# Kernel tuning notes

Measured on AMD Instinct MI355X. Metric: run time of the kernel, lower is better.

The kernel has to match this reference:

```python
import jax, jax.numpy as jnp
import numpy as np

B, T = 8, 512
ACT, EMB, DET, HID, NST = 32, 1024, 1024, 1024, 16
STO, CLS = 32, 32
UNIMIX = 0.01


def _ln(x, g, b):
    m = x.mean(-1, keepdims=True)
    v = x.var(-1, keepdims=True)
    return (x - m) / jnp.sqrt(v + 1e-5) * g + b


def _lnsilu(x, g, b):
    return jax.nn.silu(_ln(x, g, b))


def setup_inputs() -> dict:
    key = jax.random.key(0)
    ks = iter(jax.random.split(key, 40))

    def lin(din, dout):
        return jax.random.normal(next(ks), (din, dout), jnp.float32) / np.sqrt(din)

    actions = jax.random.normal(next(ks), (B, T, ACT), jnp.float32)
    embeds = jax.random.normal(next(ks), (B, T, EMB), jnp.float32)
    # pre_ssm: Linear(ACT,HID) + LayerNormSiLU(HID)
    W_pre, b_pre = lin(ACT, HID), jnp.zeros(HID)
    g_pre, bb_pre = jnp.ones(HID), jnp.zeros(HID)
    W_emb = lin(EMB, HID)  # bias=False
    W_in, b_in = lin(HID, 2 * DET), jnp.zeros(2 * DET)
    W_dt = lin(DET, DET)
    # dt bias init: inverse-softplus of dt ~ LogUniform(1e-3, 0.1)
    u = jax.random.uniform(next(ks), (DET,), jnp.float32)
    dt_init = jnp.exp(u * (np.log(0.1) - np.log(1e-3)) + np.log(1e-3))
    b_dt = dt_init + jnp.log(-jnp.expm1(-dt_init))
    W_B, W_C = lin(DET, NST), lin(DET, NST)
    A_log = jnp.broadcast_to(
        jnp.log(jnp.arange(1, NST + 1, dtype=jnp.float32)), (DET, NST)
    ) + jnp.zeros((DET, NST))
    Dp = jnp.ones(DET)
    g_out, b_out = jnp.ones(DET), jnp.zeros(DET)
    # prior_net: Linear(DET,HID)+LNSiLU+Linear(HID,STO*CLS)
    W_pr1, b_pr1 = lin(DET, HID), jnp.zeros(HID)
    g_pr, bb_pr = jnp.ones(HID), jnp.zeros(HID)
    W_pr2, b_pr2 = lin(HID, STO * CLS), jnp.zeros(STO * CLS)
    # post_net: Linear(DET+EMB,HID)+LNSiLU+Linear(HID,STO*CLS)
    W_po1, b_po1 = lin(DET + EMB, HID), jnp.zeros(HID)
    g_po, bb_po = jnp.ones(HID), jnp.zeros(HID)
    W_po2, b_po2 = lin(HID, STO * CLS), jnp.zeros(STO * CLS)
    return dict(actions=actions, embeds=embeds, W_pre=W_pre, b_pre=b_pre,
                g_pre=g_pre, bb_pre=bb_pre, W_emb=W_emb, W_in=W_in, b_in=b_in,
                W_dt=W_dt, b_dt=b_dt, W_B=W_B, W_C=W_C, A_log=A_log, Dp=Dp,
                g_out=g_out, b_out=b_out, W_pr1=W_pr1, b_pr1=b_pr1, g_pr=g_pr,
                bb_pr=bb_pr, W_pr2=W_pr2, b_pr2=b_pr2, W_po1=W_po1, b_po1=b_po1,
                g_po=g_po, bb_po=bb_po, W_po2=W_po2, b_po2=b_po2)


def reference(actions, embeds, W_pre, b_pre, g_pre, bb_pre, W_emb, W_in, b_in,
              W_dt, b_dt, W_B, W_C, A_log, Dp, g_out, b_out, W_pr1, b_pr1,
              g_pr, bb_pr, W_pr2, b_pr2, W_po1, b_po1, g_po, bb_po, W_po2, b_po2):
    # input projections
    x = _lnsilu(actions @ W_pre + b_pre, g_pre, bb_pre) + embeds @ W_emb  # (B,T,HID)
    x = x.transpose(1, 0, 2)  # (T,B,HID)
    xz = x @ W_in + b_in
    x_ssm, x_gate = xz[..., :DET], xz[..., DET:]
    dt = jax.nn.softplus(x_ssm @ W_dt + b_dt)        # (T,B,DET)
    Bp = x_ssm @ W_B                                  # (T,B,NST)
    Cp = x_ssm @ W_C                                  # (T,B,NST)
    A = -jnp.exp(A_log)                               # (DET,NST)
    gates = jnp.exp(dt[..., None] * A)                # (T,B,DET,NST)
    values = (dt * x_ssm)[..., None] * Bp[:, :, None, :]

    # linear recurrence h[t] = g[t]*h[t-1] + v[t] via associative scan
    def comb(a, c):
        g1, v1 = a
        g2, v2 = c
        return (g1 * g2, g2 * v1 + v2)

    _, h = jax.lax.associative_scan(comb, (gates, values), axis=0)
    y = jnp.einsum('tbdn,tbn->tbd', h, Cp) + Dp * x_ssm
    y = y * jax.nn.silu(x_gate)
    deter = _ln(y, g_out, b_out)                      # (T,B,DET)

    # prior / post heads
    prior = _lnsilu(deter @ W_pr1 + b_pr1, g_pr, bb_pr) @ W_pr2 + b_pr2
    emb_t = embeds.transpose(1, 0, 2)
    post_in = jnp.concatenate([deter, emb_t], -1)
    post = _lnsilu(post_in @ W_po1 + b_po1, g_po, bb_po) @ W_po2 + b_po2
    # unimix transform of post logits (deterministic part of _categorical)
    p = jax.nn.softmax(post.reshape(T, B, STO, CLS), -1)
    p = (1.0 - UNIMIX) * p + UNIMIX / CLS
    post_u = jnp.log(p + 1e-8).reshape(T, B, STO * CLS)
    return jnp.concatenate([deter, prior, post_u], -1)  # (T,B,DET+2*STO*CLS)
```

## Files before the change

kernel.cpp:

```cpp
#include <hip/hip_runtime.h>
#include <hip/hip_bf16.h>
#include <math.h>


typedef __bf16 bf16_t;
typedef __bf16 bf16x8 __attribute__((ext_vector_type(8)));
typedef float f32x4 __attribute__((ext_vector_type(4)));

#define B_   8
#define T_   512
#define R_   4096
#define HID_ 1024
#define NC_  16
#define CL_  32

static __device__ __forceinline__ float bf2f(bf16_t x) { return (float)x; }
static __device__ __forceinline__ bf16_t f2bf(float x) { return (bf16_t)x; }

typedef __attribute__((address_space(3))) unsigned int lds_u32;
typedef const __attribute__((address_space(1))) unsigned int glb_u32;
static __device__ __forceinline__ void gld16(const bf16_t* g, bf16_t* l) {
  __builtin_amdgcn_global_load_lds((glb_u32*)g, (lds_u32*)l, 16, 0, 0);
}

__global__ void detect_k(const unsigned int* __restrict__ dp_raw, int* __restrict__ flag) {
  if (threadIdx.x == 0) *flag = (dp_raw[0] == 0x3F803F80u) ? 1 : 0;
}

struct CvtArgs {
  const void* src[21];
  float* dst[21];
  int n[21];
};
__global__ __launch_bounds__(256) void cvt_vecs(CvtArgs a, const int* __restrict__ flag) {
  const bool isb = (*flag != 0);
  int v = blockIdx.y;
  const void* s = a.src[v];
  float* d = a.dst[v];
  int n = a.n[v];
  for (int i = blockIdx.x * 256 + threadIdx.x; i < n; i += 64 * 256)
    d[i] = isb ? bf2f(((const bf16_t*)s)[i]) : ((const float*)s)[i];
}

__device__ __forceinline__ void block_sum2(float& s, float& ss) {
#pragma unroll
  for (int off = 32; off > 0; off >>= 1) {
    s  += __shfl_down(s, off, 64);
    ss += __shfl_down(ss, off, 64);
  }
  __shared__ float red[8];
  int tid = threadIdx.x;
  int wave = tid >> 6, lane = tid & 63;
  if (lane == 0) { red[wave] = s; red[4 + wave] = ss; }
  __syncthreads();
  s  = red[0] + red[1] + red[2] + red[3];
  ss = red[4] + red[5] + red[6] + red[7];
}

__global__ void transpose_any(const void* __restrict__ src, bf16_t* __restrict__ dst,
                              int K, int N, const int* __restrict__ flag) {
  __shared__ float tile[32][33];
  const bool isb = (*flag != 0);
  int n0 = blockIdx.x * 32, k0 = blockIdx.y * 32;
  int tx = threadIdx.x, ty = threadIdx.y;
#pragma unroll
  for (int i = 0; i < 4; ++i) {
    size_t idx = (size_t)(k0 + ty + i * 8) * N + n0 + tx;
    tile[ty + i * 8][tx] = isb ? bf2f(((const bf16_t*)src)[idx]) : ((const float*)src)[idx];
  }
  __syncthreads();
#pragma unroll
  for (int i = 0; i < 4; ++i)
    dst[(size_t)(n0 + ty + i * 8) * K + k0 + tx] = f2bf(tile[tx][ty + i * 8]);
}

__global__ __launch_bounds__(256) void bc_build(const float* __restrict__ WB_f,
                                                const float* __restrict__ WC_f,
                                                bf16_t* __restrict__ WTbc) {
  int idx = blockIdx.x * 256 + threadIdx.x;
  int r = idx >> 10, k = idx & 1023;
  float v = 0.f;
  if (r < 16)      v = WB_f[k * 16 + r];
  else if (r < 32) v = WC_f[k * 16 + (r - 16)];
  WTbc[(size_t)r * 1024 + k] = f2bf(v);
}

__global__ __launch_bounds__(256) void reorder_emb(const void* __restrict__ emb,
                                                   bf16_t* __restrict__ embT,
                                                   const int* __restrict__ flag) {
  const bool isb = (*flag != 0);
  int r = blockIdx.x, tid = threadIdx.x;
  int t = r >> 3, b = r & 7;
  size_t base = (size_t)(b * T_ + t) * 1024;
#pragma unroll
  for (int i = 0; i < 4; ++i) {
    int c = i * 256 + tid;
    float v = isb ? bf2f(((const bf16_t*)emb)[base + c]) : ((const float*)emb)[base + c];
    embT[(size_t)r * 1024 + c] = f2bf(v);
  }
}

__global__ __launch_bounds__(256) void pre_kernel(
    const float* __restrict__ actions, const float* __restrict__ W_pre,
    const float* __restrict__ b_pre, const float* __restrict__ g_pre,
    const float* __restrict__ bb_pre, float* __restrict__ act_h) {
  int r = blockIdx.x, tid = threadIdx.x;
  int t = r >> 3, b = r & 7;
  __shared__ float a[32];
  if (tid < 32) a[tid] = actions[(size_t)(b * T_ + t) * 32 + tid];
  __syncthreads();
  float v[4];
  float s = 0.f, ss = 0.f;
#pragma unroll
  for (int i = 0; i < 4; ++i) {
    int n = i * 256 + tid;
    float acc = b_pre[n];
#pragma unroll
    for (int k = 0; k < 32; ++k) acc += a[k] * W_pre[k * HID_ + n];
    v[i] = acc; s += acc; ss += acc * acc;
  }
  block_sum2(s, ss);
  float mean = s * (1.f / 1024.f);
  float var  = ss * (1.f / 1024.f) - mean * mean;
  float rstd = rsqrtf(var + 1e-5f);
#pragma unroll
  for (int i = 0; i < 4; ++i) {
    int n = i * 256 + tid;
    float y = (v[i] - mean) * rstd * g_pre[n] + bb_pre[n];
    y = y / (1.f + __expf(-y));
    act_h[(size_t)r * HID_ + n] = y;
  }
}

enum { EPI_ADD_BF16 = 0, EPI_XZ = 1, EPI_SOFTPLUS = 2, EPI_BIAS_F32 = 3,
       EPI_PRIOR = 4, EPI_BC = 5 };

struct GemmArgs {
  const bf16_t* A;
  const bf16_t* Bt;
  int K;
  int N;
  int bnN;
  const float* bias;
  const float* addf;
  float* outf0;
  float* outf1;
  bf16_t* outh0;
  bf16_t* outh1;
  void* outv;
  const int* flag;
};

template <int EPI>
__global__ __launch_bounds__(256) void gemm_t(GemmArgs g) {
  __shared__ __align__(16) bf16_t As[64 * 32];
  __shared__ __align__(16) bf16_t Bs[64 * 32];
  const int tid = threadIdx.x;
  const int wave = tid >> 6, lane = tid & 63;
  const int K = g.K;

  const int per = gridDim.x >> 3;
  const int idx = (blockIdx.x & 7) * per + (blockIdx.x >> 3);
  const int bm = idx / g.bnN, bn = idx % g.bnN;

  f32x4 acc[2][2] = {};

  const int srow = tid >> 2;
  const int scol = (tid & 3) * 8;
  const bf16_t* Ap = g.A  + (size_t)(bm * 64 + srow) * K + scol;
  const bf16_t* Bp = g.Bt + (size_t)(bn * 64 + srow) * K + scol;
  bf16_t* AsW = &As[tid * 8];
  bf16_t* BsW = &Bs[tid * 8];

  const int wm = (wave >> 1) * 32, wn = (wave & 1) * 32;
  const int fm = lane & 15, fk = (lane >> 4) * 8;

  for (int k0 = 0; k0 < K; k0 += 32) {
    gld16(Ap + k0, AsW);
    gld16(Bp + k0, BsW);
    __syncthreads();
    bf16x8 af[2], bfr[2];
#pragma unroll
    for (int i = 0; i < 2; ++i)
      af[i] = *(const bf16x8*)&As[(wm + i * 16 + fm) * 32 + fk];
#pragma unroll
    for (int j = 0; j < 2; ++j)
      bfr[j] = *(const bf16x8*)&Bs[(wn + j * 16 + fm) * 32 + fk];
#pragma unroll
    for (int i = 0; i < 2; ++i)
#pragma unroll
      for (int j = 0; j < 2; ++j)
        acc[i][j] = __builtin_amdgcn_mfma_f32_16x16x32_bf16(af[i], bfr[j], acc[i][j], 0, 0, 0);
    __syncthreads();
  }

  const bool out_bf = (EPI == EPI_PRIOR) ? (*g.flag != 0) : false;
  const int em = (lane >> 4) * 4, en = lane & 15;
#pragma unroll
  for (int i = 0; i < 2; ++i) {
#pragma unroll
    for (int j = 0; j < 2; ++j) {
#pragma unroll
      for (int v = 0; v < 4; ++v) {
        int row = bm * 64 + wm + i * 16 + em + v;
        int col = bn * 64 + wn + j * 16 + en;
        float x = acc[i][j][v];
        if constexpr (EPI == EPI_ADD_BF16) {
          size_t o = (size_t)row * g.N + col;
          g.outh0[o] = f2bf(x + g.addf[o]);
        } else if constexpr (EPI == EPI_XZ) {
          float val = x + g.bias[col];
          if (col < 1024) {
            size_t o = (size_t)row * 1024 + col;
            g.outf0[o] = val;
            g.outh0[o] = f2bf(val);
          } else {
            size_t o = (size_t)row * 1024 + (col - 1024);
            g.outh1[o] = f2bf(val);
          }
        } else if constexpr (EPI == EPI_SOFTPLUS) {
          float val = x + g.bias[col];
          float sp = (val > 20.f) ? val : log1pf(__expf(val));
          g.outf0[(size_t)row * 1024 + col] = sp;
        } else if constexpr (EPI == EPI_BIAS_F32) {
          g.outf0[(size_t)row * g.N + col] = x + g.bias[col];
        } else if constexpr (EPI == EPI_BC) {
          if (col < 16)      g.outf0[(size_t)row * 16 + col] = x;
          else if (col < 32) g.outf1[(size_t)row * 16 + (col - 16)] = x;
        } else {
          float val = x + g.bias[col];
          size_t o = (size_t)row * 3072 + 1024 + col;
          if (out_bf) ((bf16_t*)g.outv)[o] = f2bf(val);
          else        ((float*)g.outv)[o]  = val;
        }
      }
    }
  }
}

__global__ __launch_bounds__(256) void scan_p1(const float* __restrict__ dt,
                                               const float* __restrict__ xs,
                                               const float* __restrict__ Bp,
                                               const float* __restrict__ A_log,
                                               float* __restrict__ Gp,
                                               float* __restrict__ Hl) {
  int idx = blockIdx.x * 256 + threadIdx.x;
  int d = idx & 1023;
  int cb = idx >> 10;
  int b = cb & 7, c = cb >> 3;
  float Ad[16];
#pragma unroll
  for (int n = 0; n < 16; ++n) Ad[n] = -__expf(A_log[d * 16 + n]);
  float h[16] = {};
  float dts = 0.f;
  int r0 = c * CL_ * 8 + b;
  for (int tl = 0; tl < CL_; ++tl) {
    int r = r0 + tl * 8;
    size_t off = (size_t)r * 1024 + d;
    float dtv = dt[off], xv = xs[off];
    float dtx = dtv * xv;
    dts += dtv;
    const float4* Bp4 = (const float4*)(Bp + r * 16);
    float4 b4[4] = {Bp4[0], Bp4[1], Bp4[2], Bp4[3]};
    const float* bv = (const float*)b4;
#pragma unroll
    for (int n = 0; n < 16; ++n) {
      float gg = __expf(dtv * Ad[n]);
      h[n] = gg * h[n] + dtx * bv[n];
    }
  }
  float* gp = Gp + (size_t)idx * 16;
  float* hl = Hl + (size_t)idx * 16;
#pragma unroll
  for (int q = 0; q < 4; ++q) {
    float4 gq, hq;
    gq.x = __expf(dts * Ad[q * 4 + 0]); gq.y = __expf(dts * Ad[q * 4 + 1]);
    gq.z = __expf(dts * Ad[q * 4 + 2]); gq.w = __expf(dts * Ad[q * 4 + 3]);
    hq.x = h[q * 4 + 0]; hq.y = h[q * 4 + 1]; hq.z = h[q * 4 + 2]; hq.w = h[q * 4 + 3];
    ((float4*)gp)[q] = gq;
    ((float4*)hl)[q] = hq;
  }
}

__global__ __launch_bounds__(256) void scan_p2(float* __restrict__ GpCin,
                                               const float* __restrict__ Hl) {
  int j = blockIdx.x * 256 + threadIdx.x;
  float carry = 0.f;
#pragma unroll
  for (int c = 0; c < NC_; ++c) {
    size_t o = (size_t)c * 131072 + j;
    float gv = GpCin[o], hl = Hl[o];
    GpCin[o] = carry;
    carry = gv * carry + hl;
  }
}

__global__ __launch_bounds__(256) void scan_p3(const float* __restrict__ dt,
                                               const float* __restrict__ xs,
                                               const bf16_t* __restrict__ xg,
                                               const float* __restrict__ Bp,
                                               const float* __restrict__ Cp,
                                               const float* __restrict__ A_log,
                                               const float* __restrict__ Dp,
                                               const float* __restrict__ Cin,
                                               float* __restrict__ y) {
  int idx = blockIdx.x * 256 + threadIdx.x;
  int d = idx & 1023;
  int cb = idx >> 10;
  int b = cb & 7, c = cb >> 3;
  float Ad[16];
#pragma unroll
  for (int n = 0; n < 16; ++n) Ad[n] = -__expf(A_log[d * 16 + n]);
  float Dd = Dp[d];
  float h[16];
  const float4* Ci4 = (const float4*)(Cin + (size_t)idx * 16);
#pragma unroll
  for (int q = 0; q < 4; ++q) {
    float4 cq = Ci4[q];
    h[q * 4 + 0] = cq.x; h[q * 4 + 1] = cq.y; h[q * 4 + 2] = cq.z; h[q * 4 + 3] = cq.w;
  }
  int r0 = c * CL_ * 8 + b;
  for (int tl = 0; tl < CL_; ++tl) {
    int r = r0 + tl * 8;
    size_t off = (size_t)r * 1024 + d;
    float dtv = dt[off], xv = xs[off], gv = bf2f(xg[off]);
    float dtx = dtv * xv;
    const float4* Bp4 = (const float4*)(Bp + r * 16);
    const float4* Cp4 = (const float4*)(Cp + r * 16);
    float4 b4[4] = {Bp4[0], Bp4[1], Bp4[2], Bp4[3]};
    float4 c4[4] = {Cp4[0], Cp4[1], Cp4[2], Cp4[3]};
    const float* bv = (const float*)b4;
    const float* cv = (const float*)c4;
    float yv = 0.f;
#pragma unroll
    for (int n = 0; n < 16; ++n) {
      float gg = __expf(dtv * Ad[n]);
      h[n] = gg * h[n] + dtx * bv[n];
      yv += h[n] * cv[n];
    }
    yv += Dd * xv;
    float sg = gv / (1.f + __expf(-gv));
    y[off] = yv * sg;
  }
}

template <int MODE>
__global__ __launch_bounds__(256) void ln_k(const float* __restrict__ in,
                                            const float* __restrict__ gw,
                                            const float* __restrict__ bw,
                                            bf16_t* __restrict__ out0,
                                            void* __restrict__ out1,
                                            const int* __restrict__ flag) {
  const bool out_bf = (MODE == 0) ? (*flag != 0) : false;
  int r = blockIdx.x, tid = threadIdx.x;
  float v[4];
  float s = 0.f, ss = 0.f;
#pragma unroll
  for (int i = 0; i < 4; ++i) {
    v[i] = in[(size_t)r * 1024 + i * 256 + tid];
    s += v[i]; ss += v[i] * v[i];
  }
  block_sum2(s, ss);
  float mean = s * (1.f / 1024.f);
  float var  = ss * (1.f / 1024.f) - mean * mean;
  float rstd = rsqrtf(var + 1e-5f);
#pragma unroll
  for (int i = 0; i < 4; ++i) {
    int c = i * 256 + tid;
    float yv = (v[i] - mean) * rstd * gw[c] + bw[c];
    if constexpr (MODE == 1) yv = yv / (1.f + __expf(-yv));
    out0[(size_t)r * 1024 + c] = f2bf(yv);
    if constexpr (MODE == 0) {
      size_t o = (size_t)r * 3072 + c;
      if (out_bf) ((bf16_t*)out1)[o] = f2bf(yv);
      else        ((float*)out1)[o]  = yv;
    }
  }
}

__global__ __launch_bounds__(256) void assemble_post(const bf16_t* __restrict__ deter,
                                                     const bf16_t* __restrict__ embT,
                                                     bf16_t* __restrict__ post_in) {
  int r = blockIdx.x, tid = threadIdx.x;
  unsigned int* dst = (unsigned int*)(post_in + (size_t)r * 2048);
  const unsigned int* s0 = (const unsigned int*)(deter + (size_t)r * 1024);
  const unsigned int* s1 = (const unsigned int*)(embT + (size_t)r * 1024);
  dst[tid] = s0[tid];
  dst[256 + tid] = s0[256 + tid];
  dst[512 + tid] = s1[tid];
  dst[768 + tid] = s1[256 + tid];
}

__global__ __launch_bounds__(256) void softmax_k(const float* __restrict__ logits,
                                                 void* __restrict__ out,
                                                 const int* __restrict__ flag) {
  const bool out_bf = (*flag != 0);
  int idx = blockIdx.x * 256 + threadIdx.x;
  int r = idx >> 5, grp = idx & 31;
  const float* p = logits + (size_t)r * 1024 + grp * 32;
  float x[32];
  float m = -1e30f;
#pragma unroll
  for (int j = 0; j < 32; ++j) { x[j] = p[j]; m = fmaxf(m, x[j]); }
  float sum = 0.f;
#pragma unroll
  for (int j = 0; j < 32; ++j) { x[j] = __expf(x[j] - m); sum += x[j]; }
  float inv = 0.99f / sum;
  size_t base = (size_t)r * 3072 + 2048 + grp * 32;
#pragma unroll
  for (int j = 0; j < 32; ++j) {
    float val = logf(x[j] * inv + (0.01f / 32.f) + 1e-8f);
    if (out_bf) ((bf16_t*)out)[base + j] = f2bf(val);
    else        ((float*)out)[base + j]  = val;
  }
}

extern "C" void kernel_launch(void* const* d_in, const int* in_sizes, int n_in,
                              void* d_out, int out_size, void* d_ws, size_t ws_size,
                              hipStream_t stream) {
  (void)in_sizes; (void)n_in; (void)out_size; (void)ws_size;
  const void* actions = d_in[0];
  const void* embeds  = d_in[1];
  const void* W_pre   = d_in[2];
  const void* b_pre   = d_in[3];
  const void* g_pre   = d_in[4];
  const void* bb_pre  = d_in[5];
  const void* W_emb   = d_in[6];
  const void* W_in    = d_in[7];
  const void* b_in    = d_in[8];
  const void* W_dt    = d_in[9];
  const void* b_dt    = d_in[10];
  const void* W_B     = d_in[11];
  const void* W_C     = d_in[12];
  const void* A_log   = d_in[13];
  const void* Dp      = d_in[14];
  const void* g_out   = d_in[15];
  const void* b_out   = d_in[16];
  const void* W_pr1   = d_in[17];
  const void* b_pr1   = d_in[18];
  const void* g_pr    = d_in[19];
  const void* bb_pr   = d_in[20];
  const void* W_pr2   = d_in[21];
  const void* b_pr2   = d_in[22];
  const void* W_po1   = d_in[23];
  const void* b_po1   = d_in[24];
  const void* g_po    = d_in[25];
  const void* bb_po   = d_in[26];
  const void* W_po2   = d_in[27];
  const void* b_po2   = d_in[28];

  char* ws = (char*)d_ws;
  const size_t MB = 1ull << 20;
  const size_t KB = 1024;
  bf16_t* WTemb = (bf16_t*)(ws + 0);
  bf16_t* WTin  = (bf16_t*)(ws + 2 * MB);
  bf16_t* WTdt  = (bf16_t*)(ws + 6 * MB);
  bf16_t* WTpr1 = (bf16_t*)(ws + 8 * MB);
  bf16_t* WTpr2 = (bf16_t*)(ws + 10 * MB);
  bf16_t* WTpo1 = (bf16_t*)(ws + 12 * MB);
  bf16_t* WTpo2 = (bf16_t*)(ws + 16 * MB);
  bf16_t* embT  = (bf16_t*)(ws + 18 * MB);
  float*  F1    = (float*)(ws + 26 * MB);
  float*  F2    = (float*)(ws + 42 * MB);
  float*  F5    = (float*)(ws + 58 * MB);
  bf16_t* B8    = (bf16_t*)(ws + 74 * MB);
  bf16_t* B9    = (bf16_t*)(ws + 82 * MB);
  bf16_t* G8    = (bf16_t*)(ws + 90 * MB);
  float*  BpB   = (float*)(ws + 98 * MB);
  float*  CpB   = (float*)(ws + 98 * MB + 256 * KB);
  float*  Hl    = (float*)(ws + 0);
  float*  Gp    = (float*)(ws + 74 * MB);
  char* cb = ws + 98 * MB + 512 * KB;
  int*   flag    = (int*)(cb);                cb += 256;
  float* act_f   = (float*)(cb);              cb += 131072 * 4;
  float* Wpre_f  = (float*)(cb);              cb += 32768 * 4;
  float* WB_f    = (float*)(cb);              cb += 16384 * 4;
  float* WC_f    = (float*)(cb);              cb += 16384 * 4;
  float* Alog_f  = (float*)(cb);              cb += 16384 * 4;
  float* Dp_f    = (float*)(cb);              cb += 1024 * 4;
  float* bpre_f  = (float*)(cb);              cb += 1024 * 4;
  float* gpre_f  = (float*)(cb);              cb += 1024 * 4;
  float* bbpre_f = (float*)(cb);              cb += 1024 * 4;
  float* bin_f   = (float*)(cb);              cb += 2048 * 4;
  float* bdt_f   = (float*)(cb);              cb += 1024 * 4;
  float* gout_f  = (float*)(cb);              cb += 1024 * 4;
  float* bout_f  = (float*)(cb);              cb += 1024 * 4;
  float* bpr1_f  = (float*)(cb);              cb += 1024 * 4;
  float* gpr_f   = (float*)(cb);              cb += 1024 * 4;
  float* bbpr_f  = (float*)(cb);              cb += 1024 * 4;
  float* bpr2_f  = (float*)(cb);              cb += 1024 * 4;
  float* bpo1_f  = (float*)(cb);              cb += 1024 * 4;
  float* gpo_f   = (float*)(cb);              cb += 1024 * 4;
  float* bbpo_f  = (float*)(cb);              cb += 1024 * 4;
  float* bpo2_f  = (float*)(cb);              cb += 1024 * 4;
  bf16_t* WTbc   = (bf16_t*)(cb);             cb += 64 * 1024 * 2;

  detect_k<<<1, 64, 0, stream>>>((const unsigned int*)Dp, flag);

  CvtArgs ca{};
  const void* srcs[21] = {actions, W_pre, W_B, W_C, A_log, Dp, b_pre, g_pre, bb_pre,
                          b_in, b_dt, g_out, b_out, b_pr1, g_pr, bb_pr, b_pr2,
                          b_po1, g_po, bb_po, b_po2};
  float* dsts[21] = {act_f, Wpre_f, WB_f, WC_f, Alog_f, Dp_f, bpre_f, gpre_f, bbpre_f,
                     bin_f, bdt_f, gout_f, bout_f, bpr1_f, gpr_f, bbpr_f, bpr2_f,
                     bpo1_f, gpo_f, bbpo_f, bpo2_f};
  int ns[21] = {131072, 32768, 16384, 16384, 16384, 1024, 1024, 1024, 1024,
                2048, 1024, 1024, 1024, 1024, 1024, 1024, 1024,
                1024, 1024, 1024, 1024};
  for (int i = 0; i < 21; ++i) { ca.src[i] = srcs[i]; ca.dst[i] = dsts[i]; ca.n[i] = ns[i]; }
  cvt_vecs<<<dim3(64, 21), 256, 0, stream>>>(ca, flag);

  dim3 tb(32, 8);
  transpose_any<<<dim3(32, 32), tb, 0, stream>>>(W_emb, WTemb, 1024, 1024, flag);
  transpose_any<<<dim3(64, 32), tb, 0, stream>>>(W_in,  WTin,  1024, 2048, flag);
  transpose_any<<<dim3(32, 32), tb, 0, stream>>>(W_dt,  WTdt,  1024, 1024, flag);
  transpose_any<<<dim3(32, 32), tb, 0, stream>>>(W_pr1, WTpr1, 1024, 1024, flag);
  transpose_any<<<dim3(32, 32), tb, 0, stream>>>(W_pr2, WTpr2, 1024, 1024, flag);
  transpose_any<<<dim3(32, 64), tb, 0, stream>>>(W_po1, WTpo1, 2048, 1024, flag);
  transpose_any<<<dim3(32, 32), tb, 0, stream>>>(W_po2, WTpo2, 1024, 1024, flag);
  bc_build<<<256, 256, 0, stream>>>(WB_f, WC_f, WTbc);

  reorder_emb<<<R_, 256, 0, stream>>>(embeds, embT, flag);
  pre_kernel<<<R_, 256, 0, stream>>>(act_f, Wpre_f, bpre_f, gpre_f, bbpre_f, F1);

  {
    GemmArgs a{}; a.A = embT; a.Bt = WTemb; a.K = 1024; a.N = 1024; a.bnN = 16;
    a.addf = F1; a.outh0 = B8;
    gemm_t<EPI_ADD_BF16><<<1024, 256, 0, stream>>>(a);
  }
  {
    GemmArgs a{}; a.A = B8; a.Bt = WTin; a.K = 1024; a.N = 2048; a.bnN = 32;
    a.bias = bin_f; a.outf0 = F2; a.outh0 = B9; a.outh1 = G8;
    gemm_t<EPI_XZ><<<2048, 256, 0, stream>>>(a);
  }
  {
    GemmArgs a{}; a.A = B9; a.Bt = WTbc; a.K = 1024; a.N = 64; a.bnN = 1;
    a.outf0 = BpB; a.outf1 = CpB;
    gemm_t<EPI_BC><<<64, 256, 0, stream>>>(a);
  }
  {
    GemmArgs a{}; a.A = B9; a.Bt = WTdt; a.K = 1024; a.N = 1024; a.bnN = 16;
    a.bias = bdt_f; a.outf0 = F1;
    gemm_t<EPI_SOFTPLUS><<<1024, 256, 0, stream>>>(a);
  }
  scan_p1<<<512, 256, 0, stream>>>(F1, F2, BpB, Alog_f, Gp, Hl);
  scan_p2<<<512, 256, 0, stream>>>(Gp, Hl);
  scan_p3<<<512, 256, 0, stream>>>(F1, F2, G8, BpB, CpB, Alog_f, Dp_f, Gp, F5);
  ln_k<0><<<R_, 256, 0, stream>>>(F5, gout_f, bout_f, B9, d_out, flag);
  {
    GemmArgs a{}; a.A = B9; a.Bt = WTpr1; a.K = 1024; a.N = 1024; a.bnN = 16;
    a.bias = bpr1_f; a.outf0 = F1;
    gemm_t<EPI_BIAS_F32><<<1024, 256, 0, stream>>>(a);
  }
  ln_k<1><<<R_, 256, 0, stream>>>(F1, gpr_f, bbpr_f, B8, nullptr, flag);
  {
    GemmArgs a{}; a.A = B8; a.Bt = WTpr2; a.K = 1024; a.N = 1024; a.bnN = 16;
    a.bias = bpr2_f; a.outv = d_out; a.flag = flag;
    gemm_t<EPI_PRIOR><<<1024, 256, 0, stream>>>(a);
  }
  assemble_post<<<R_, 256, 0, stream>>>(B9, embT, (bf16_t*)F5);
  {
    GemmArgs a{}; a.A = (bf16_t*)F5; a.Bt = WTpo1; a.K = 2048; a.N = 1024; a.bnN = 16;
    a.bias = bpo1_f; a.outf0 = F2;
    gemm_t<EPI_BIAS_F32><<<1024, 256, 0, stream>>>(a);
  }
  ln_k<1><<<R_, 256, 0, stream>>>(F2, gpo_f, bbpo_f, B8, nullptr, flag);
  {
    GemmArgs a{}; a.A = B8; a.Bt = WTpo2; a.K = 1024; a.N = 1024; a.bnN = 16;
    a.bias = bpo2_f; a.outf0 = F1;
    gemm_t<EPI_BIAS_F32><<<1024, 256, 0, stream>>>(a);
  }
  softmax_k<<<512, 256, 0, stream>>>(F1, d_out, flag);
}
```

Baseline: 530.8 us.

## Batch weight transposes, drop fp32 staging copies, and re-chunk the scan

Merges the seven transpose launches into one batched kernel with per-matrix tile offsets. pre_kernel and bc_build now read raw inputs through a dtype-aware loader, so the fp32 conversion of actions and weights is dropped and cvt_vecs gets fewer, smaller grids. The scan chunking is changed (NC/CL swapped, scan_p1 and scan_p3 use twice as many blocks) and the Hl buffer is moved so it no longer aliases the weight workspace. These aim to cut launch overhead and scan latency, but the scan geometry change depends on code that is not visible here.

```diff
diff --git a/kernel.cpp b/kernel.cpp
--- a/kernel.cpp
+++ b/kernel.cpp
@@ -11,11 +11,14 @@
 #define T_   512
 #define R_   4096
 #define HID_ 1024
-#define NC_  16
-#define CL_  32
+#define NC_  32
+#define CL_  16
 
 static __device__ __forceinline__ float bf2f(bf16_t x) { return (float)x; }
 static __device__ __forceinline__ bf16_t f2bf(float x) { return (bf16_t)x; }
+static __device__ __forceinline__ float ldany(const void* p, size_t i, bool isb) {
+  return isb ? bf2f(((const bf16_t*)p)[i]) : ((const float*)p)[i];
+}
 
 typedef __attribute__((address_space(3))) unsigned int lds_u32;
 typedef const __attribute__((address_space(1))) unsigned int glb_u32;
@@ -28,9 +31,9 @@
 }
 
 struct CvtArgs {
-  const void* src[21];
-  float* dst[21];
-  int n[21];
+  const void* src[17];
+  float* dst[17];
+  int n[17];
 };
 __global__ __launch_bounds__(256) void cvt_vecs(CvtArgs a, const int* __restrict__ flag) {
   const bool isb = (*flag != 0);
@@ -38,8 +41,8 @@
   const void* s = a.src[v];
   float* d = a.dst[v];
   int n = a.n[v];
-  for (int i = blockIdx.x * 256 + threadIdx.x; i < n; i += 64 * 256)
-    d[i] = isb ? bf2f(((const bf16_t*)s)[i]) : ((const float*)s)[i];
+  for (int i = blockIdx.x * 256 + threadIdx.x; i < n; i += 8 * 256)
+    d[i] = ldany(s, i, isb);
 }
 
 __device__ __forceinline__ void block_sum2(float& s, float& ss) {
@@ -57,16 +60,30 @@
   ss = red[4] + red[5] + red[6] + red[7];
 }
 
-__global__ void transpose_any(const void* __restrict__ src, bf16_t* __restrict__ dst,
-                              int K, int N, const int* __restrict__ flag) {
+struct TrArgs {
+  const void* src[7];
+  bf16_t* dst[7];
+  int K[7], N[7];
+  int tile0[8];
+};
+__global__ void tr_batch(TrArgs a, const int* __restrict__ flag) {
   __shared__ float tile[32][33];
   const bool isb = (*flag != 0);
-  int n0 = blockIdx.x * 32, k0 = blockIdx.y * 32;
+  int bid = blockIdx.x;
+  int m = 0;
+#pragma unroll
+  for (int q = 0; q < 6; ++q) if (bid >= a.tile0[q + 1]) m = q + 1;
+  int local = bid - a.tile0[m];
+  int K = a.K[m], N = a.N[m];
+  int ntx = N >> 5;
+  int n0 = (local % ntx) * 32, k0 = (local / ntx) * 32;
+  const void* src = a.src[m];
+  bf16_t* dst = a.dst[m];
   int tx = threadIdx.x, ty = threadIdx.y;
 #pragma unroll
   for (int i = 0; i < 4; ++i) {
     size_t idx = (size_t)(k0 + ty + i * 8) * N + n0 + tx;
-    tile[ty + i * 8][tx] = isb ? bf2f(((const bf16_t*)src)[idx]) : ((const float*)src)[idx];
+    tile[ty + i * 8][tx] = ldany(src, idx, isb);
   }
   __syncthreads();
 #pragma unroll
@@ -74,14 +91,16 @@
     dst[(size_t)(n0 + ty + i * 8) * K + k0 + tx] = f2bf(tile[tx][ty + i * 8]);
 }
 
-__global__ __launch_bounds__(256) void bc_build(const float* __restrict__ WB_f,
-                                                const float* __restrict__ WC_f,
-                                                bf16_t* __restrict__ WTbc) {
+__global__ __launch_bounds__(256) void bc_build(const void* __restrict__ W_B,
+                                                const void* __restrict__ W_C,
+                                                bf16_t* __restrict__ WTbc,
+                                                const int* __restrict__ flag) {
+  const bool isb = (*flag != 0);
   int idx = blockIdx.x * 256 + threadIdx.x;
   int r = idx >> 10, k = idx & 1023;
   float v = 0.f;
-  if (r < 16)      v = WB_f[k * 16 + r];
-  else if (r < 32) v = WC_f[k * 16 + (r - 16)];
+  if (r < 16)      v = ldany(W_B, k * 16 + r, isb);
+  else if (r < 32) v = ldany(W_C, k * 16 + (r - 16), isb);
   WTbc[(size_t)r * 1024 + k] = f2bf(v);
 }
 
@@ -95,19 +114,20 @@
 #pragma unroll
   for (int i = 0; i < 4; ++i) {
     int c = i * 256 + tid;
-    float v = isb ? bf2f(((const bf16_t*)emb)[base + c]) : ((const float*)emb)[base + c];
-    embT[(size_t)r * 1024 + c] = f2bf(v);
+    embT[(size_t)r * 1024 + c] = f2bf(ldany(emb, base + c, isb));
   }
 }
 
 __global__ __launch_bounds__(256) void pre_kernel(
-    const float* __restrict__ actions, const float* __restrict__ W_pre,
+    const void* __restrict__ actions, const void* __restrict__ W_pre,
     const float* __restrict__ b_pre, const float* __restrict__ g_pre,
-    const float* __restrict__ bb_pre, float* __restrict__ act_h) {
+    const float* __restrict__ bb_pre, float* __restrict__ act_h,
+    const int* __restrict__ flag) {
+  const bool isb = (*flag != 0);
   int r = blockIdx.x, tid = threadIdx.x;
   int t = r >> 3, b = r & 7;
   __shared__ float a[32];
-  if (tid < 32) a[tid] = actions[(size_t)(b * T_ + t) * 32 + tid];
+  if (tid < 32) a[tid] = ldany(actions, (size_t)(b * T_ + t) * 32 + tid, isb);
   __syncthreads();
   float v[4];
   float s = 0.f, ss = 0.f;
@@ -116,7 +136,7 @@
     int n = i * 256 + tid;
     float acc = b_pre[n];
 #pragma unroll
-    for (int k = 0; k < 32; ++k) acc += a[k] * W_pre[k * HID_ + n];
+    for (int k = 0; k < 32; ++k) acc += a[k] * ldany(W_pre, k * HID_ + n, isb);
     v[i] = acc; s += acc; ss += acc * acc;
   }
   block_sum2(s, ss);
@@ -468,14 +488,10 @@
   bf16_t* G8    = (bf16_t*)(ws + 90 * MB);
   float*  BpB   = (float*)(ws + 98 * MB);
   float*  CpB   = (float*)(ws + 98 * MB + 256 * KB);
-  float*  Hl    = (float*)(ws + 0);
+  float*  Hl    = (float*)(ws + 58 * MB);
   float*  Gp    = (float*)(ws + 74 * MB);
   char* cb = ws + 98 * MB + 512 * KB;
   int*   flag    = (int*)(cb);                cb += 256;
-  float* act_f   = (float*)(cb);              cb += 131072 * 4;
-  float* Wpre_f  = (float*)(cb);              cb += 32768 * 4;
-  float* WB_f    = (float*)(cb);              cb += 16384 * 4;
-  float* WC_f    = (float*)(cb);              cb += 16384 * 4;
   float* Alog_f  = (float*)(cb);              cb += 16384 * 4;
   float* Dp_f    = (float*)(cb);              cb += 1024 * 4;
   float* bpre_f  = (float*)(cb);              cb += 1024 * 4;
@@ -498,30 +514,36 @@
   detect_k<<<1, 64, 0, stream>>>((const unsigned int*)Dp, flag);
 
   CvtArgs ca{};
-  const void* srcs[21] = {actions, W_pre, W_B, W_C, A_log, Dp, b_pre, g_pre, bb_pre,
-                          b_in, b_dt, g_out, b_out, b_pr1, g_pr, bb_pr, b_pr2,
+  const void* srcs[17] = {A_log, Dp, b_pre, g_pre, bb_pre, b_in, b_dt,
+                          g_out, b_out, b_pr1, g_pr, bb_pr, b_pr2,
                           b_po1, g_po, bb_po, b_po2};
-  float* dsts[21] = {act_f, Wpre_f, WB_f, WC_f, Alog_f, Dp_f, bpre_f, gpre_f, bbpre_f,
-                     bin_f, bdt_f, gout_f, bout_f, bpr1_f, gpr_f, bbpr_f, bpr2_f,
+  float* dsts[17] = {Alog_f, Dp_f, bpre_f, gpre_f, bbpre_f, bin_f, bdt_f,
+                     gout_f, bout_f, bpr1_f, gpr_f, bbpr_f, bpr2_f,
                      bpo1_f, gpo_f, bbpo_f, bpo2_f};
-  int ns[21] = {131072, 32768, 16384, 16384, 16384, 1024, 1024, 1024, 1024,
-                2048, 1024, 1024, 1024, 1024, 1024, 1024, 1024,
+  int ns[17] = {16384, 1024, 1024, 1024, 1024, 2048, 1024,
+                1024, 1024, 1024, 1024, 1024, 1024,
                 1024, 1024, 1024, 1024};
-  for (int i = 0; i < 21; ++i) { ca.src[i] = srcs[i]; ca.dst[i] = dsts[i]; ca.n[i] = ns[i]; }
-  cvt_vecs<<<dim3(64, 21), 256, 0, stream>>>(ca, flag);
-
-  dim3 tb(32, 8);
-  transpose_any<<<dim3(32, 32), tb, 0, stream>>>(W_emb, WTemb, 1024, 1024, flag);
-  transpose_any<<<dim3(64, 32), tb, 0, stream>>>(W_in,  WTin,  1024, 2048, flag);
-  transpose_any<<<dim3(32, 32), tb, 0, stream>>>(W_dt,  WTdt,  1024, 1024, flag);
-  transpose_any<<<dim3(32, 32), tb, 0, stream>>>(W_pr1, WTpr1, 1024, 1024, flag);
-  transpose_any<<<dim3(32, 32), tb, 0, stream>>>(W_pr2, WTpr2, 1024, 1024, flag);
-  transpose_any<<<dim3(32, 64), tb, 0, stream>>>(W_po1, WTpo1, 2048, 1024, flag);
-  transpose_any<<<dim3(32, 32), tb, 0, stream>>>(W_po2, WTpo2, 1024, 1024, flag);
-  bc_build<<<256, 256, 0, stream>>>(WB_f, WC_f, WTbc);
+  for (int i = 0; i < 17; ++i) { ca.src[i] = srcs[i]; ca.dst[i] = dsts[i]; ca.n[i] = ns[i]; }
+  cvt_vecs<<<dim3(8, 17), 256, 0, stream>>>(ca, flag);
+
+  {
+    TrArgs ta{};
+    const void* tsrc[7] = {W_emb, W_in, W_dt, W_pr1, W_pr2, W_po1, W_po2};
+    bf16_t* tdst[7] = {WTemb, WTin, WTdt, WTpr1, WTpr2, WTpo1, WTpo2};
+    int tK[7] = {1024, 1024, 1024, 1024, 1024, 2048, 1024};
+    int tN[7] = {1024, 2048, 1024, 1024, 1024, 1024, 1024};
+    int off = 0;
+    for (int i = 0; i < 7; ++i) {
+      ta.src[i] = tsrc[i]; ta.dst[i] = tdst[i]; ta.K[i] = tK[i]; ta.N[i] = tN[i];
+      ta.tile0[i] = off; off += (tK[i] >> 5) * (tN[i] >> 5);
+    }
+    ta.tile0[7] = off;
+    tr_batch<<<off, dim3(32, 8), 0, stream>>>(ta, flag);
+  }
+  bc_build<<<256, 256, 0, stream>>>(W_B, W_C, WTbc, flag);
 
   reorder_emb<<<R_, 256, 0, stream>>>(embeds, embT, flag);
-  pre_kernel<<<R_, 256, 0, stream>>>(act_f, Wpre_f, bpre_f, gpre_f, bbpre_f, F1);
+  pre_kernel<<<R_, 256, 0, stream>>>(actions, W_pre, bpre_f, gpre_f, bbpre_f, F1, flag);
 
   {
     GemmArgs a{}; a.A = embT; a.Bt = WTemb; a.K = 1024; a.N = 1024; a.bnN = 16;
@@ -543,9 +565,9 @@
     a.bias = bdt_f; a.outf0 = F1;
     gemm_t<EPI_SOFTPLUS><<<1024, 256, 0, stream>>>(a);
   }
-  scan_p1<<<512, 256, 0, stream>>>(F1, F2, BpB, Alog_f, Gp, Hl);
+  scan_p1<<<1024, 256, 0, stream>>>(F1, F2, BpB, Alog_f, Gp, Hl);
   scan_p2<<<512, 256, 0, stream>>>(Gp, Hl);
-  scan_p3<<<512, 256, 0, stream>>>(F1, F2, G8, BpB, CpB, Alog_f, Dp_f, Gp, F5);
+  scan_p3<<<1024, 256, 0, stream>>>(F1, F2, G8, BpB, CpB, Alog_f, Dp_f, Gp, F5);
   ln_k<0><<<R_, 256, 0, stream>>>(F5, gout_f, bout_f, B9, d_out, flag);
   {
     GemmArgs a{}; a.A = B9; a.Bt = WTpr1; a.K = 1024; a.N = 1024; a.bnN = 16;
```

Result: no change. 535.9 us (+0.9%).
